# Kernel optimization log

Hardware: AMD Instinct MI355X
Metric: run time of the kernel (lower is better)

Reference implementation:

```python
import jax, jax.numpy as jnp
import numpy as np

B, N, D = 2, 2048, 1024
H = 16
HD = D // H  # 64
N_CTX = 256


def setup_inputs() -> dict:
    key = jax.random.key(0)
    ks = jax.random.split(key, 10)
    x = jax.random.normal(ks[0], (B, N, D), dtype=jnp.float32)
    ctx_ppr = jax.random.uniform(ks[1], (N_CTX,), dtype=jnp.float32, minval=1e-4, maxval=1.0)
    ctx_trust = jax.random.uniform(ks[2], (N_CTX,), dtype=jnp.float32)
    attn_mask = jax.random.randint(ks[3], (N, N), 0, 2).astype(jnp.bool_)
    # parameters (nn.Linear convention: y = x @ W.T + b)
    s_in = 1.0 / np.sqrt(D)
    W_in = jax.random.uniform(ks[4], (3 * D, D), dtype=jnp.float32, minval=-s_in, maxval=s_in)
    b_in = jax.random.uniform(ks[5], (3 * D,), dtype=jnp.float32, minval=-s_in, maxval=s_in)
    W_out = jax.random.uniform(ks[6], (D, D), dtype=jnp.float32, minval=-s_in, maxval=s_in)
    b_out = jax.random.uniform(ks[7], (D,), dtype=jnp.float32, minval=-s_in, maxval=s_in)
    log_ppr_alpha = jnp.ones((1,), jnp.float32) * 0.1
    trust_scale = jnp.ones((1,), jnp.float32) * 0.1
    return {"x": x, "ctx_ppr": ctx_ppr, "ctx_trust": ctx_trust, "n_ctx": N_CTX,
            "attn_mask": attn_mask, "W_in": W_in, "b_in": b_in,
            "W_out": W_out, "b_out": b_out,
            "log_ppr_alpha": log_ppr_alpha, "trust_scale": trust_scale}


def reference(x, ctx_ppr, ctx_trust, n_ctx, attn_mask, W_in, b_in, W_out, b_out,
              log_ppr_alpha, trust_scale):
    Bx, Nx, Dx = x.shape
    scale = HD ** -0.5
    qkv = x @ W_in.T + b_in  # [B,N,3D]
    q, k, v = jnp.split(qkv, 3, axis=-1)
    q = q.reshape(Bx, Nx, H, HD).transpose(0, 2, 1, 3)  # [B,H,N,d]
    k = k.reshape(Bx, Nx, H, HD).transpose(0, 2, 1, 3)
    v = v.reshape(Bx, Nx, H, HD).transpose(0, 2, 1, 3)
    if n_ctx > 0:
        gate = jax.nn.sigmoid(trust_scale[0] * ctx_trust)  # [n_ctx]
        gate_full = jnp.concatenate([gate, jnp.ones(Nx - n_ctx, x.dtype)])
        v = v * gate_full[None, None, :, None]
    logits = jnp.einsum('bhqd,bhkd->bhqk', q, k) * scale
    if n_ctx > 0:
        bias = log_ppr_alpha[0] * jnp.log(jnp.clip(ctx_ppr, 1e-8, None))
        col_bias = jnp.concatenate([bias, jnp.zeros(Nx - n_ctx, x.dtype)])
        logits = logits + col_bias[None, None, None, :]
    logits = jnp.where(attn_mask[None, None, :, :], -jnp.inf, logits)
    weights = jax.nn.softmax(logits, axis=-1)
    out = jnp.einsum('bhqk,bhkd->bhqd', weights, v)
    out = out.transpose(0, 2, 1, 3).reshape(Bx, Nx, Dx)
    return out @ W_out.T + b_out
```

## Files before the change

kernel.cpp:

```cpp
#include <hip/hip_runtime.h>
#include <hip/hip_bf16.h>
#include <math.h>

#define B_   2
#define N_   2048
#define D_   1024
#define H_   16
#define TD_  3072
#define LOG2E 1.44269504088896340736f
#define SCALE_Q (0.125f * LOG2E)

typedef short  bf16x8 __attribute__((ext_vector_type(8)));
typedef _Float16 f16x8 __attribute__((ext_vector_type(8)));
typedef _Float16 f16x4 __attribute__((ext_vector_type(4)));
typedef float  f32x4  __attribute__((ext_vector_type(4)));
typedef float  f32x16 __attribute__((ext_vector_type(16)));

#define MFMA32B(a, b, c)  __builtin_amdgcn_mfma_f32_32x32x16_bf16(a, b, c, 0, 0, 0)
#define MFMA32H(a, b, c)  __builtin_amdgcn_mfma_f32_32x32x16_f16(a, b, c, 0, 0, 0)

__device__ __forceinline__ ushort f2bf(float f) {
    union { float f; unsigned u; } v; v.f = f;
    unsigned r = (v.u + 0x7fffu + ((v.u >> 16) & 1u)) >> 16;
    return (ushort)r;
}
__device__ __forceinline__ unsigned pkrtz(float a, float b) {
    typedef __fp16 h2 __attribute__((ext_vector_type(2)));
    union { h2 h; unsigned u; } c;
    c.h = __builtin_amdgcn_cvt_pkrtz(a, b);
    return c.u;
}
__device__ __forceinline__ void async16(const void* g, void* l) {
    __builtin_amdgcn_global_load_lds(
        (const __attribute__((address_space(1))) unsigned*)g,
        (__attribute__((address_space(3))) unsigned*)l, 16, 0, 0);
}
__device__ __forceinline__ void plswap(unsigned &a, unsigned &b) {
    auto r = __builtin_amdgcn_permlane32_swap((int)a, (int)b, false, false);
    a = (unsigned)r[0]; b = (unsigned)r[1];
}

__global__ __launch_bounds__(256) void preprocess(
    const float* __restrict__ x, const float* __restrict__ W_in,
    const float* __restrict__ W_out, const float* __restrict__ ctx_ppr,
    const float* __restrict__ log_alpha, const int* __restrict__ n_ctx_p,
    const int* __restrict__ mask,
    ushort* __restrict__ xb, ushort* __restrict__ wib, ushort* __restrict__ wob,
    float* __restrict__ biasrow, unsigned* __restrict__ maskbits)
{
    const int J0 = 1048576, J1 = 786432, J2 = 262144, JM = 131072, JB = 2048;
    int t = blockIdx.x * 256 + threadIdx.x;
    if (t < J0 + J1 + J2) {
        const float* src; ushort* dst; int i = t;
        if (i < J0)           { src = x;      dst = xb;  }
        else if (i < J0 + J1) { i -= J0;      src = W_in;  dst = wib; }
        else                  { i -= J0 + J1; src = W_out; dst = wob; }
        float4 v = ((const float4*)src)[i];
        ushort4 o;
        o.x = f2bf(v.x); o.y = f2bf(v.y); o.z = f2bf(v.z); o.w = f2bf(v.w);
        ((ushort4*)dst)[i] = o;
    } else if (t < J0 + J1 + J2 + JM) {
        int i = t - (J0 + J1 + J2);
        const int4* m = (const int4*)(mask + (size_t)i * 32);
        unsigned bits = 0u;
        #pragma unroll
        for (int j = 0; j < 8; ++j) {
            int4 w = m[j];
            bits |= (w.x != 0 ? 1u : 0u) << (j * 4 + 0);
            bits |= (w.y != 0 ? 1u : 0u) << (j * 4 + 1);
            bits |= (w.z != 0 ? 1u : 0u) << (j * 4 + 2);
            bits |= (w.w != 0 ? 1u : 0u) << (j * 4 + 3);
        }
        maskbits[i] = bits;
    } else if (t < J0 + J1 + J2 + JM + JB) {
        int k = t - (J0 + J1 + J2 + JM);
        int nc = n_ctx_p[0];
        float bv = 0.f;
        if (k < nc) bv = log_alpha[0] * __log2f(fmaxf(ctx_ppr[k], 1e-8f));
        biasrow[k] = bv;
    }
}

template<int BCOL, int MODE>
__global__ __launch_bounds__(256) void gemm32(
    const ushort* __restrict__ A, const ushort* __restrict__ Bw,
    const float* __restrict__ bias, float* __restrict__ Cout,
    ushort* __restrict__ qkout, _Float16* __restrict__ vTout,
    int Ncol, int K,
    const float* __restrict__ ctx_trust, const float* __restrict__ trust_scale,
    const int* __restrict__ n_ctx_p)
{
    constexpr int CT = BCOL / 64;
    constexpr int LB = BCOL / 32;
    constexpr int NCP = (MODE == 1 ? 3072 : 1024) / BCOL;
    constexpr int NWG = NCP * 32;
    constexpr int CHUNK = NWG / 8;
    __shared__ ushort tA[2][128 * 64];
    __shared__ ushort tB[2][BCOL * 64];
    const int tid = threadIdx.x;
    const int lane = tid & 63, wv = tid >> 6;
    const int q31 = lane & 31, hi = lane >> 5;
    const int rh = wv >> 1, ch = wv & 1;
    const int id = blockIdx.x;
    const int wg = (id & 7) * CHUNK + (id >> 3);
    const int row0 = (wg / NCP) * 128, col0 = (wg % NCP) * BCOL;

    const int swz = q31 & 7;
    int offAr[2], offBr[CT];
    #pragma unroll
    for (int rt = 0; rt < 2; ++rt) offAr[rt] = (rh * 64 + rt * 32 + q31) * 64;
    #pragma unroll
    for (int ct = 0; ct < CT; ++ct) offBr[ct] = (ch * (BCOL / 2) + ct * 32 + q31) * 64;

    f32x16 acc[2][CT];
    #pragma unroll
    for (int i = 0; i < 2; ++i)
        #pragma unroll
        for (int j = 0; j < CT; ++j) acc[i][j] = (f32x16)(0.f);

    int arow[4], asg[4], brow[LB], bsg[LB];
    #pragma unroll
    for (int r2 = 0; r2 < 4; ++r2) {
        int g = r2 * 256 + tid;
        arow[r2] = g >> 3; asg[r2] = ((g & 7) ^ ((g >> 3) & 7)) << 3;
    }
    #pragma unroll
    for (int r2 = 0; r2 < LB; ++r2) {
        int g = r2 * 256 + tid;
        brow[r2] = g >> 3; bsg[r2] = ((g & 7) ^ ((g >> 3) & 7)) << 3;
    }
    const ushort* Ab = A + (size_t)row0 * K;
    const ushort* Bb = Bw + (size_t)col0 * K;

    auto issue = [&](int ktile, int bufi) {
        const int kt = ktile * 64;
        #pragma unroll
        for (int r2 = 0; r2 < 4; ++r2)
            async16(Ab + (size_t)arow[r2] * K + kt + asg[r2],
                    &tA[bufi][(r2 * 256 + tid) * 8]);
        #pragma unroll
        for (int r2 = 0; r2 < LB; ++r2)
            async16(Bb + (size_t)brow[r2] * K + kt + bsg[r2],
                    &tB[bufi][(r2 * 256 + tid) * 8]);
    };

    issue(0, 0);
    const int NIT = K / 64;
    #pragma unroll 1
    for (int it = 0; it < NIT; ++it) {
        const int cur = it & 1;
        asm volatile("s_barrier" ::: "memory");
        if (it + 1 < NIT) {
            issue(it + 1, cur ^ 1);
            if constexpr (BCOL == 192)
                asm volatile("s_waitcnt vmcnt(10)" ::: "memory");
            else if constexpr (BCOL == 128)
                asm volatile("s_waitcnt vmcnt(8)" ::: "memory");
            else
                asm volatile("s_waitcnt vmcnt(6)" ::: "memory");
        } else {
            asm volatile("s_waitcnt vmcnt(0)" ::: "memory");
        }
        asm volatile("s_barrier" ::: "memory");

        const ushort* KA = tA[cur];
        const ushort* KB = tB[cur];
        __builtin_amdgcn_s_setprio(1);
        #pragma unroll
        for (int kk = 0; kk < 4; ++kk) {
            const int gr = ((kk * 2 + hi) ^ swz) << 3;
            bf16x8 af[2], bfv[CT];
            #pragma unroll
            for (int rt = 0; rt < 2; ++rt)
                af[rt] = *(const bf16x8*)&KA[offAr[rt] + gr];
            #pragma unroll
            for (int ct = 0; ct < CT; ++ct)
                bfv[ct] = *(const bf16x8*)&KB[offBr[ct] + gr];
            #pragma unroll
            for (int rt = 0; rt < 2; ++rt)
                #pragma unroll
                for (int ct = 0; ct < CT; ++ct)
                    acc[rt][ct] = MFMA32B(af[rt], bfv[ct], acc[rt][ct]);
        }
        __builtin_amdgcn_s_setprio(0);
    }

    const int nctx = n_ctx_p ? n_ctx_p[0] : 0;
    const float ts = trust_scale ? trust_scale[0] : 0.f;
    #pragma unroll
    for (int ct = 0; ct < CT; ++ct) {
        const int col = col0 + ch * (BCOL / 2) + ct * 32 + q31;
        const float bv = bias[col];
        #pragma unroll
        for (int rt = 0; rt < 2; ++rt) {
            const int rb0 = row0 + rh * 64 + rt * 32 + 4 * hi;
            f32x16 a = acc[rt][ct];
            if (MODE == 0) {
                #pragma unroll
                for (int g2 = 0; g2 < 4; ++g2)
                    #pragma unroll
                    for (int r = 0; r < 4; ++r)
                        Cout[(size_t)(rb0 + 8 * g2 + r) * Ncol + col] = a[g2 * 4 + r] + bv;
            } else if (col < D_) {
                #pragma unroll
                for (int g2 = 0; g2 < 4; ++g2)
                    #pragma unroll
                    for (int r = 0; r < 4; ++r)
                        qkout[(size_t)(rb0 + 8 * g2 + r) * 2048 + col] =
                            f2bf((a[g2 * 4 + r] + bv) * SCALE_Q);
            } else if (col < 2 * D_) {
                #pragma unroll
                for (int g2 = 0; g2 < 4; ++g2)
                    #pragma unroll
                    for (int r = 0; r < 4; ++r)
                        qkout[(size_t)(rb0 + 8 * g2 + r) * 2048 + col] =
                            f2bf(a[g2 * 4 + r] + bv);
            } else {
                const int vc = col - 2 * D_;
                const int hh = vc >> 6, dim = vc & 63;
                const int bb = row0 >> 11;
                #pragma unroll
                for (int g2 = 0; g2 < 4; ++g2) {
                    const int nbase = (rb0 + 8 * g2) & (N_ - 1);
                    ushort4 o;
                    #pragma unroll
                    for (int r = 0; r < 4; ++r) {
                        float v = a[g2 * 4 + r] + bv;
                        const int n = nbase + r;
                        if (n < nctx)
                            v *= 1.f / (1.f + __expf(-ts * ctx_trust[n]));
                        _Float16 hv = (_Float16)v;
                        ((ushort*)&o)[r] = *(ushort*)&hv;
                    }
                    *(ushort4*)&vTout[((size_t)(bb * 16 + hh) * 64 + dim) * 2048 + nbase] = o;
                }
            }
        }
    }
}

__global__ __launch_bounds__(256, 4) void attn(
    const ushort* __restrict__ qkb,
    const _Float16* __restrict__ vT,
    const unsigned* __restrict__ maskbits,
    const float* __restrict__ biasrow,
    const int* __restrict__ n_ctx_p,
    _Float16* __restrict__ op0,
    _Float16* __restrict__ op1,
    float* __restrict__ lpart)
{
    __shared__ ushort   Kt[3][64 * 64];
    __shared__ _Float16 Vt[2][64 * 64];
    const int tid = threadIdx.x;
    const int lane = tid & 63, wv = tid >> 6;
    const int q31 = lane & 31, hi = lane >> 5;
    const int b = blockIdx.y >> 4, h = blockIdx.y & 15;
    const int q0w = blockIdx.x * 128 + wv * 32;
    const int kh = blockIdx.z;
    const int kbase = kh << 10;
    const int nctx = n_ctx_p[0];

    const int lin = blockIdx.x + (blockIdx.y << 4) + (blockIdx.z << 9);
    const int rot = ((lin >> 8) << 2) & 15;

    union fi { float f; int i; };
    fi ng; ng.f = -1e30f;
    const int NEGI = ng.i;

    bf16x8 qf[4];
    {
        const ushort* qrow = qkb + (size_t)(b * N_ + q0w + q31) * 2048 + h * 64;
        #pragma unroll
        for (int ks = 0; ks < 4; ++ks)
            qf[ks] = *(const bf16x8*)(qrow + ks * 16 + hi * 8);
    }
    const size_t kgbase = (size_t)(b * N_ + kbase) * 2048 + 1024 + h * 64;
    const _Float16* vbase = vT + (size_t)((b * 16 + h) * 64) * 2048 + kbase;
    const unsigned* mrow = maskbits + (size_t)(q0w + q31) * 64 + (kbase >> 5);

    int goff[2], ldso[2];
    #pragma unroll
    for (int r2 = 0; r2 < 2; ++r2) {
        int g = r2 * 256 + tid, row = g >> 3, sg = (g & 7) ^ (row & 7);
        goff[r2] = row * 2048 + sg * 8;
        ldso[r2] = g * 8;
    }

    f32x16 O[2];
    O[0] = (f32x16)(0.f); O[1] = (f32x16)(0.f);
    float lrun = 0.f;

    const int cp0 = rot, cp1 = (rot + 1) & 15;
    uint2 mcur = *(const uint2*)&mrow[cp0 * 2];
    asm volatile("" ::: "memory");
    {
        const ushort* gp0 = qkb + kgbase + (size_t)cp0 * (64 * 2048);
        #pragma unroll
        for (int r2 = 0; r2 < 2; ++r2) async16(gp0 + goff[r2], &Kt[0][ldso[r2]]);
        const _Float16* vp = vbase + cp0 * 64;
        #pragma unroll
        for (int r2 = 0; r2 < 2; ++r2) async16(vp + goff[r2], &Vt[0][ldso[r2]]);
        const ushort* gp1 = qkb + kgbase + (size_t)cp1 * (64 * 2048);
        #pragma unroll
        for (int r2 = 0; r2 < 2; ++r2) async16(gp1 + goff[r2], &Kt[1][ldso[r2]]);
    }

    const int swz = q31 & 7;
    int kb = 0;
    #pragma unroll 1
    for (int ci = 0; ci < 16; ++ci) {
        asm volatile("s_barrier" ::: "memory");
        uint2 mnext = mcur;
        if (ci < 15) {
            const int cpv = (ci + 1 + rot) & 15;
            mnext = *(const uint2*)&mrow[cpv * 2];
            asm volatile("" ::: "memory");
            const _Float16* vp = vbase + cpv * 64;
            #pragma unroll
            for (int r2 = 0; r2 < 2; ++r2)
                async16(vp + goff[r2], &Vt[(ci + 1) & 1][ldso[r2]]);
        }
        if (ci < 14) {
            int nb = kb + 2; if (nb >= 3) nb -= 3;
            const int cpk = (ci + 2 + rot) & 15;
            const ushort* gp = qkb + kgbase + (size_t)cpk * (64 * 2048);
            #pragma unroll
            for (int r2 = 0; r2 < 2; ++r2)
                async16(gp + goff[r2], &Kt[nb][ldso[r2]]);
        }
        if (ci < 14)       asm volatile("s_waitcnt vmcnt(7)" ::: "memory");
        else if (ci == 14) asm volatile("s_waitcnt vmcnt(5)" ::: "memory");
        else               asm volatile("s_waitcnt vmcnt(0)" ::: "memory");
        asm volatile("s_barrier" ::: "memory");

        const ushort*   KT = Kt[kb];
        const _Float16* VT = Vt[ci & 1];
        const int cp = (ci + rot) & 15;
        const int c0g = kbase + cp * 64;
        const bool has_bias = (c0g < nctx);
        float lsum = 0.f;

        #pragma unroll
        for (int t = 0; t < 2; ++t) {
            f32x16 S = (f32x16)(0.f);
            const int rbase = (t * 32 + q31) * 64;
            __builtin_amdgcn_s_setprio(1);
            #pragma unroll
            for (int ks = 0; ks < 4; ++ks) {
                bf16x8 kf = *(const bf16x8*)&KT[rbase + (((ks * 2 + hi) ^ swz) << 3)];
                S = MFMA32B(kf, qf[ks], S);
            }
            __builtin_amdgcn_s_setprio(0);

            const unsigned msh = (t ? mcur.y : mcur.x) >> (hi * 4);
            unsigned pk[8];
            float lt = 0.f;
            #pragma unroll
            for (int g = 0; g < 4; ++g) {
                f32x4 bb;
                if (has_bias)
                    bb = *(const f32x4*)&biasrow[c0g + t * 32 + g * 8 + hi * 4];
                float pr[4];
                #pragma unroll
                for (int r = 0; r < 4; ++r) {
                    const int br = r + 8 * g;
                    float s = S[g * 4 + r];
                    if (has_bias) s += bb[r];
                    int mi = ((int)(msh << (31 - br))) >> 31;
                    fi su; su.f = s;
                    su.i = (mi & NEGI) | (su.i & ~mi);
                    pr[r] = __builtin_amdgcn_exp2f(su.f);
                }
                lt += (pr[0] + pr[1]) + (pr[2] + pr[3]);
                pk[g * 2 + 0] = pkrtz(pr[0], pr[1]);
                pk[g * 2 + 1] = pkrtz(pr[2], pr[3]);
            }
            lsum += lt;

            __builtin_amdgcn_s_setprio(1);
            #pragma unroll
            for (int kss = 0; kss < 2; ++kss) {
                const int ks = 2 * t + kss, lo4 = kss * 4;
                unsigned w0 = pk[lo4 + 0], w1 = pk[lo4 + 1];
                unsigned w2 = pk[lo4 + 2], w3 = pk[lo4 + 3];
                plswap(w0, w2);
                plswap(w1, w3);
                union { f16x8 v; unsigned u[4]; } frag;
                frag.u[0] = w0; frag.u[1] = w1;
                frag.u[2] = w2; frag.u[3] = w3;
                #pragma unroll
                for (int t2 = 0; t2 < 2; ++t2) {
                    const int vb = (t2 * 32 + q31) * 64;
                    union { f16x8 v; int4 i4; } vf;
                    vf.i4 = *(const int4*)&VT[vb + (((ks * 2 + hi) ^ swz) << 3)];
                    O[t2] = MFMA32H(vf.v, frag.v, O[t2]);
                }
            }
            __builtin_amdgcn_s_setprio(0);
        }
        lrun += lsum;
        mcur = mnext;
        kb = kb + 1; if (kb >= 3) kb -= 3;
    }

    float l = lrun + __shfl_xor(lrun, 32);
    float inv = 1.f / l;
    _Float16* orow = (kh ? op1 : op0)
                   + (size_t)(b * N_ + q0w + q31) * 1024 + h * 64;
    #pragma unroll
    for (int t = 0; t < 2; ++t)
        #pragma unroll
        for (int g = 0; g < 4; ++g) {
            ushort4 o;
            #pragma unroll
            for (int r = 0; r < 4; ++r) {
                _Float16 hv = (_Float16)(O[t][g * 4 + r] * inv);
                ((ushort*)&o)[r] = *(ushort*)&hv;
            }
            *(ushort4*)&orow[t * 32 + g * 8 + hi * 4] = o;
        }
    if (hi == 0)
        lpart[(kh << 16) + (b * 16 + h) * 2048 + q0w + q31] = l;
}

__global__ __launch_bounds__(256) void combine(
    const _Float16* __restrict__ op0, const _Float16* __restrict__ op1,
    const float* __restrict__ lpart, ushort* __restrict__ attb)
{
    int t = blockIdx.x * 256 + threadIdx.x;
    size_t idx = (size_t)t * 4;
    int col = (int)(idx & 1023);
    int row = (int)(idx >> 10);
    int h = col >> 6;
    int b = row >> 11, q = row & 2047;
    int lidx = (b * 16 + h) * 2048 + q;
    float l0 = lpart[lidx], l1 = lpart[65536 + lidx];
    float inv = 1.f / (l0 + l1);
    float w0 = l0 * inv, w1 = l1 * inv;
    f16x4 a0 = *(const f16x4*)(op0 + idx);
    f16x4 a1 = *(const f16x4*)(op1 + idx);
    ushort4 o;
    #pragma unroll
    for (int r = 0; r < 4; ++r)
        ((ushort*)&o)[r] = f2bf((float)a0[r] * w0 + (float)a1[r] * w1);
    *(ushort4*)(attb + idx) = o;
}

extern "C" void kernel_launch(void* const* d_in, const int* in_sizes, int n_in,
                              void* d_out, int out_size, void* d_ws, size_t ws_size,
                              hipStream_t stream)
{
    const float* x         = (const float*)d_in[0];
    const float* ctx_ppr   = (const float*)d_in[1];
    const float* ctx_trust = (const float*)d_in[2];
    const int*   n_ctx_p   = (const int*)d_in[3];
    const int*   attn_mask = (const int*)d_in[4];
    const float* W_in      = (const float*)d_in[5];
    const float* b_in      = (const float*)d_in[6];
    const float* W_out     = (const float*)d_in[7];
    const float* b_out     = (const float*)d_in[8];
    const float* log_alpha = (const float*)d_in[9];
    const float* trust_sc  = (const float*)d_in[10];
    float* out = (float*)d_out;

    char* ws = (char*)d_ws;
    ushort*    xb       = (ushort*)ws;    ws += (size_t)4096 * 1024 * 2;
    ushort*    wib      = (ushort*)ws;    ws += (size_t)3072 * 1024 * 2;
    ushort*    wob      = (ushort*)ws;    ws += (size_t)1024 * 1024 * 2;
    ushort*    qkb      = (ushort*)ws;    ws += (size_t)4096 * 2048 * 2;
    _Float16*  vT       = (_Float16*)ws;  ws += (size_t)2048 * 2048 * 2;
    ushort*    attbuf   = (ushort*)ws;    ws += (size_t)4096 * 1024 * 2;
    float*     biasrow  = (float*)ws;     ws += 2048 * 4;
    unsigned*  maskbits = (unsigned*)ws;  ws += (size_t)2048 * 64 * 4;

    _Float16* op0   = (_Float16*)xb;
    _Float16* op1   = (_Float16*)attbuf;
    float*    lpart = (float*)wib;

    hipLaunchKernelGGL(preprocess, dim3(8712), dim3(256), 0, stream,
                       x, W_in, W_out, ctx_ppr, log_alpha, n_ctx_p, attn_mask,
                       xb, wib, wob, biasrow, maskbits);

    hipLaunchKernelGGL((gemm32<192, 1>), dim3(512), dim3(256), 0, stream,
                       xb, wib, b_in, (float*)nullptr, qkb, vT, TD_, 1024,
                       ctx_trust, trust_sc, n_ctx_p);

    hipLaunchKernelGGL(attn, dim3(16, 32, 2), dim3(256), 0, stream,
                       qkb, vT, maskbits, biasrow, n_ctx_p, op0, op1, lpart);

    hipLaunchKernelGGL(combine, dim3(4096), dim3(256), 0, stream,
                       op0, op1, lpart, attbuf);

    hipLaunchKernelGGL((gemm32<128, 0>), dim3(256), dim3(256), 0, stream,
                       attbuf, wob, b_out, out, (ushort*)nullptr, (_Float16*)nullptr,
                       1024, 1024, ctx_trust, trust_sc, n_ctx_p);
}
```

Before: 250.1 us.

## Use 128-key tiles with double-buffered K/V in attention and narrower output GEMM tile

The attention kernel now processes 128-key chunks per iteration, 8 iterations instead of 16, with simple double buffering of K and V tiles. This replaces the triple-buffered K and double-buffered V scheme, and the V swizzle and mask-word handling are adjusted to the wider tile. The goal is fewer barriers and loop iterations per block. In exchange, shared memory per block roughly doubles and launch bounds drop to 2 blocks per CU, which lowers occupancy and shortens the prefetch lookahead. Separately, the output projection GEMM switches to a 64-wide tile with twice the grid, to fill more CUs.

```diff
diff --git a/kernel.cpp b/kernel.cpp
--- a/kernel.cpp
+++ b/kernel.cpp
@@ -239,7 +239,7 @@
     }
 }
 
-__global__ __launch_bounds__(256, 4) void attn(
+__global__ __launch_bounds__(256, 2) void attn(
     const ushort* __restrict__ qkb,
     const _Float16* __restrict__ vT,
     const unsigned* __restrict__ maskbits,
@@ -249,8 +249,8 @@
     _Float16* __restrict__ op1,
     float* __restrict__ lpart)
 {
-    __shared__ ushort   Kt[3][64 * 64];
-    __shared__ _Float16 Vt[2][64 * 64];
+    __shared__ ushort   Kt[2][128 * 64];
+    __shared__ _Float16 Vt[2][64 * 128];
     const int tid = threadIdx.x;
     const int lane = tid & 63, wv = tid >> 6;
     const int q31 = lane & 31, hi = lane >> 5;
@@ -261,7 +261,7 @@
     const int nctx = n_ctx_p[0];
 
     const int lin = blockIdx.x + (blockIdx.y << 4) + (blockIdx.z << 9);
-    const int rot = ((lin >> 8) << 2) & 15;
+    const int rot = ((lin >> 8) << 1) & 7;
 
     union fi { float f; int i; };
     fi ng; ng.f = -1e30f;
@@ -278,11 +278,14 @@
     const _Float16* vbase = vT + (size_t)((b * 16 + h) * 64) * 2048 + kbase;
     const unsigned* mrow = maskbits + (size_t)(q0w + q31) * 64 + (kbase >> 5);
 
-    int goff[2], ldso[2];
-    #pragma unroll
-    for (int r2 = 0; r2 < 2; ++r2) {
-        int g = r2 * 256 + tid, row = g >> 3, sg = (g & 7) ^ (row & 7);
-        goff[r2] = row * 2048 + sg * 8;
+    int goffK[4], goffV[4], ldso[4];
+    #pragma unroll
+    for (int r2 = 0; r2 < 4; ++r2) {
+        int g = r2 * 256 + tid;
+        int rK = g >> 3, sK = (g & 7) ^ (rK & 7);
+        goffK[r2] = rK * 2048 + sK * 8;
+        int rV = g >> 4, sV = (g & 15) ^ (rV & 7);
+        goffV[r2] = rV * 2048 + sV * 8;
         ldso[r2] = g * 8;
     }
 
@@ -290,58 +293,51 @@
     O[0] = (f32x16)(0.f); O[1] = (f32x16)(0.f);
     float lrun = 0.f;
 
-    const int cp0 = rot, cp1 = (rot + 1) & 15;
-    uint2 mcur = *(const uint2*)&mrow[cp0 * 2];
+    const int cp0 = rot;
+    uint4 mcur = *(const uint4*)&mrow[cp0 * 4];
     asm volatile("" ::: "memory");
     {
-        const ushort* gp0 = qkb + kgbase + (size_t)cp0 * (64 * 2048);
-        #pragma unroll
-        for (int r2 = 0; r2 < 2; ++r2) async16(gp0 + goff[r2], &Kt[0][ldso[r2]]);
-        const _Float16* vp = vbase + cp0 * 64;
-        #pragma unroll
-        for (int r2 = 0; r2 < 2; ++r2) async16(vp + goff[r2], &Vt[0][ldso[r2]]);
-        const ushort* gp1 = qkb + kgbase + (size_t)cp1 * (64 * 2048);
-        #pragma unroll
-        for (int r2 = 0; r2 < 2; ++r2) async16(gp1 + goff[r2], &Kt[1][ldso[r2]]);
+        const ushort* gp = qkb + kgbase + (size_t)cp0 * (128 * 2048);
+        #pragma unroll
+        for (int r2 = 0; r2 < 4; ++r2) async16(gp + goffK[r2], &Kt[0][ldso[r2]]);
+        const _Float16* vp = vbase + cp0 * 128;
+        #pragma unroll
+        for (int r2 = 0; r2 < 4; ++r2) async16(vp + goffV[r2], &Vt[0][ldso[r2]]);
     }
 
     const int swz = q31 & 7;
-    int kb = 0;
     #pragma unroll 1
-    for (int ci = 0; ci < 16; ++ci) {
+    for (int ci = 0; ci < 8; ++ci) {
         asm volatile("s_barrier" ::: "memory");
-        uint2 mnext = mcur;
-        if (ci < 15) {
-            const int cpv = (ci + 1 + rot) & 15;
-            mnext = *(const uint2*)&mrow[cpv * 2];
+        uint4 mnext = mcur;
+        if (ci < 7) {
+            const int cpn = (ci + 1 + rot) & 7;
+            mnext = *(const uint4*)&mrow[cpn * 4];
             asm volatile("" ::: "memory");
-            const _Float16* vp = vbase + cpv * 64;
-            #pragma unroll
-            for (int r2 = 0; r2 < 2; ++r2)
-                async16(vp + goff[r2], &Vt[(ci + 1) & 1][ldso[r2]]);
-        }
-        if (ci < 14) {
-            int nb = kb + 2; if (nb >= 3) nb -= 3;
-            const int cpk = (ci + 2 + rot) & 15;
-            const ushort* gp = qkb + kgbase + (size_t)cpk * (64 * 2048);
-            #pragma unroll
-            for (int r2 = 0; r2 < 2; ++r2)
-                async16(gp + goff[r2], &Kt[nb][ldso[r2]]);
-        }
-        if (ci < 14)       asm volatile("s_waitcnt vmcnt(7)" ::: "memory");
-        else if (ci == 14) asm volatile("s_waitcnt vmcnt(5)" ::: "memory");
-        else               asm volatile("s_waitcnt vmcnt(0)" ::: "memory");
+            const ushort* gp = qkb + kgbase + (size_t)cpn * (128 * 2048);
+            #pragma unroll
+            for (int r2 = 0; r2 < 4; ++r2)
+                async16(gp + goffK[r2], &Kt[(ci + 1) & 1][ldso[r2]]);
+            const _Float16* vp = vbase + cpn * 128;
+            #pragma unroll
+            for (int r2 = 0; r2 < 4; ++r2)
+                async16(vp + goffV[r2], &Vt[(ci + 1) & 1][ldso[r2]]);
+            asm volatile("s_waitcnt vmcnt(9)" ::: "memory");
+        } else {
+            asm volatile("s_waitcnt vmcnt(0)" ::: "memory");
+        }
         asm volatile("s_barrier" ::: "memory");
 
-        const ushort*   KT = Kt[kb];
+        const ushort*   KT = Kt[ci & 1];
         const _Float16* VT = Vt[ci & 1];
-        const int cp = (ci + rot) & 15;
-        const int c0g = kbase + cp * 64;
+        const int cp = (ci + rot) & 7;
+        const int c0g = kbase + cp * 128;
         const bool has_bias = (c0g < nctx);
+        const unsigned mw[4] = { mcur.x, mcur.y, mcur.z, mcur.w };
         float lsum = 0.f;
 
         #pragma unroll
-        for (int t = 0; t < 2; ++t) {
+        for (int t = 0; t < 4; ++t) {
             f32x16 S = (f32x16)(0.f);
             const int rbase = (t * 32 + q31) * 64;
             __builtin_amdgcn_s_setprio(1);
@@ -352,7 +348,7 @@
             }
             __builtin_amdgcn_s_setprio(0);
 
-            const unsigned msh = (t ? mcur.y : mcur.x) >> (hi * 4);
+            const unsigned msh = mw[t] >> (hi * 4);
             unsigned pk[8];
             float lt = 0.f;
             #pragma unroll
@@ -380,7 +376,7 @@
             __builtin_amdgcn_s_setprio(1);
             #pragma unroll
             for (int kss = 0; kss < 2; ++kss) {
-                const int ks = 2 * t + kss, lo4 = kss * 4;
+                const int lo4 = kss * 4;
                 unsigned w0 = pk[lo4 + 0], w1 = pk[lo4 + 1];
                 unsigned w2 = pk[lo4 + 2], w3 = pk[lo4 + 3];
                 plswap(w0, w2);
@@ -388,11 +384,12 @@
                 union { f16x8 v; unsigned u[4]; } frag;
                 frag.u[0] = w0; frag.u[1] = w1;
                 frag.u[2] = w2; frag.u[3] = w3;
+                const int vslot = ((t * 4 + kss * 2 + hi) ^ swz) << 3;
                 #pragma unroll
                 for (int t2 = 0; t2 < 2; ++t2) {
-                    const int vb = (t2 * 32 + q31) * 64;
+                    const int vb = (t2 * 32 + q31) * 128;
                     union { f16x8 v; int4 i4; } vf;
-                    vf.i4 = *(const int4*)&VT[vb + (((ks * 2 + hi) ^ swz) << 3)];
+                    vf.i4 = *(const int4*)&VT[vb + vslot];
                     O[t2] = MFMA32H(vf.v, frag.v, O[t2]);
                 }
             }
@@ -400,7 +397,6 @@
         }
         lrun += lsum;
         mcur = mnext;
-        kb = kb + 1; if (kb >= 3) kb -= 3;
     }
 
     float l = lrun + __shfl_xor(lrun, 32);
@@ -491,7 +487,7 @@
     hipLaunchKernelGGL(combine, dim3(4096), dim3(256), 0, stream,
                        op0, op1, lpart, attbuf);
 
-    hipLaunchKernelGGL((gemm32<128, 0>), dim3(256), dim3(256), 0, stream,
+    hipLaunchKernelGGL((gemm32<64, 0>), dim3(512), dim3(256), 0, stream,
                        attbuf, wob, b_out, out, (ushort*)nullptr, (_Float16*)nullptr,
                        1024, 1024, ctx_trust, trust_sc, n_ctx_p);
 }
```

Result: slower. 256.8 us (+2.7%).
